# Optimization experiments

Measured on AMD Instinct MI355X. Metric: run time of the kernel, lower is better.

## Reference

```python
import jax, jax.numpy as jnp
import numpy as np

FEATS = 768
HEAD = 12
HD = FEATS // HEAD  # 64
B, N = 128, 197


def setup_inputs() -> dict:
    key = jax.random.key(0)
    k0, k1, k2 = jax.random.split(key, 3)
    x = jax.random.normal(k0, (B, N, FEATS), dtype=jnp.float32)
    W_qkv = jax.random.normal(k1, (HEAD, HD, 3 * HD), dtype=jnp.float32) * 0.05
    b_qkv = jnp.zeros((HEAD, 3 * HD), dtype=jnp.float32)
    # out_dim_3dk: Linear(feats -> feats)
    W_out = jax.random.normal(k2, (FEATS, FEATS), dtype=jnp.float32) * 0.02
    b_out = jnp.zeros((FEATS,), dtype=jnp.float32)
    return {"x": x, "W_qkv": W_qkv, "b_qkv": b_qkv, "W_out": W_out, "b_out": b_out}


def reference(x, W_qkv, b_qkv, W_out, b_out):
    b, n, f = x.shape
    h, hd = W_qkv.shape[0], W_qkv.shape[1]
    # x.chunk(head, dim=2) == reshape into per-head feature slices
    xh = x.reshape(b, n, h, hd)
    # per-head Linear(hd -> 3*hd): hX_dim_3dk
    qkv = jnp.einsum('bnhd,hde->bnhe', xh, W_qkv) + b_qkv  # [b,n,h,3*hd]
    q, k, v = jnp.split(qkv, 3, axis=-1)  # each [b,n,h,hd]
    # NOTE: original scales by sqrt(feats), not sqrt(head_dim)
    scale = jnp.asarray(f, x.dtype) ** 0.5
    scores = jnp.einsum('bihd,bjhd->bhij', q, k) / scale  # [b,h,n,n]
    p = jax.nn.softmax(scores, axis=-1)
    attn = jnp.einsum('bhij,bjhd->bihd', p, v)  # [b,n,h,hd]
    # concat head outputs along feature dim, then out_dim_3dk
    out = attn.reshape(b, n, f) @ W_out + b_out
    return out  # dropout p=0.0 is identity
```

## Files before the change

### kernel.cpp

```cpp
#include <hip/hip_runtime.h>
#include <hip/hip_bf16.h>

#define FEATS 768
#define HEADS 12
#define HD    64
#define BB    128
#define NN    197
#define M_TOT (BB * NN)
#define SCALE_INV (3.6084391824351615e-02f)
#define VS    216

typedef __bf16 bf16x8 __attribute__((ext_vector_type(8)));
typedef float  f32x4  __attribute__((ext_vector_type(4)));
typedef unsigned short u16x8 __attribute__((ext_vector_type(8)));

__device__ __forceinline__ unsigned short f2bf1(float f) {
    __bf16 h = (__bf16)f;
    return *(unsigned short*)&h;
}
__device__ __forceinline__ unsigned int f2bf2(float lo, float hi) {
    return (unsigned int)f2bf1(lo) | ((unsigned int)f2bf1(hi) << 16);
}

__global__ __launch_bounds__(256) void prep_kernel(
    const float* __restrict__ Wqkv, unsigned short* __restrict__ Wt_sw,
    const float* __restrict__ W,    unsigned short* __restrict__ Wt)
{
    __shared__ __align__(16) char plds[49152];
    const int t = threadIdx.x;
    if (blockIdx.x < 12) {
        float* wl = (float*)plds;
        const int h = blockIdx.x;
        const float* Wh = Wqkv + (long)h * (64 * 192);
        for (int i = t; i < 64 * 192; i += 256) wl[i] = Wh[i];
        __syncthreads();
        for (int c = t; c < 1536; c += 256) {
            int row = c >> 3, kc = (c & 7) ^ (row & 7);
            u16x8 v;
            #pragma unroll
            for (int j = 0; j < 8; ++j) v[j] = f2bf1(wl[(kc * 8 + j) * 192 + row]);
            *(u16x8*)&Wt_sw[(long)h * 12288 + c * 8] = v;
        }
    } else {
        float (*tile)[33] = (float(*)[33])plds;
        const int idx = blockIdx.x - 12;
        const int kb = (idx % 24) * 32, nb = (idx / 24) * 32;
        const int tx = t & 31, ty = t >> 5;
        for (int r = ty; r < 32; r += 8)
            tile[r][tx] = W[(long)(kb + r) * FEATS + nb + tx];
        __syncthreads();
        for (int r = ty; r < 32; r += 8) {
            const int n = nb + r, k = kb + tx;
            const long phys = (long)n * FEATS + ((k >> 6) << 6)
                            + ((((k >> 3) & 7) ^ (n & 7)) << 3) + (k & 7);
            Wt[phys] = f2bf1(tile[tx][r]);
        }
    }
}

__global__ __launch_bounds__(512, 4) void qkv_attn_fused(
    const float* __restrict__ x, const unsigned short* __restrict__ Wt_sw,
    const float* __restrict__ bqkv, unsigned short* __restrict__ attn)
{
    __shared__ __align__(16) char lds[80912];
    unsigned short* As  = (unsigned short*)lds;
    unsigned short* Ws  = (unsigned short*)(lds + 26624);
    unsigned short* Ql  = (unsigned short*)lds;
    unsigned short* Kl  = (unsigned short*)(lds + 26624);
    unsigned short* Vtl = (unsigned short*)(lds + 53248);
    unsigned short* Pl  = (unsigned short*)lds;

    const int t  = threadIdx.x;
    const int w  = t >> 6, l = t & 63;
    const int lr = l & 15, g = l >> 4, g4 = g * 4;
    const int b  = blockIdx.x, h = blockIdx.y;

    {
        const uint4 z = {0, 0, 0, 0};
        #pragma unroll
        for (int it = 0; it < 4; ++it) {
            int idx = it * 512 + t;
            if (idx < 1729) *(uint4*)&Vtl[idx * 8] = z;
        }
    }
    #pragma unroll
    for (int it = 0; it < 4; ++it) {
        int p = it * 512 + t;
        if (p < 1664) {
            int row = p >> 3, kc = (p & 7) ^ (row & 7);
            uint4 pk = {0, 0, 0, 0};
            if (row < NN) {
                const float* src = x + ((long)b * NN + row) * FEATS + h * HD + kc * 8;
                const float4 x0 = *(const float4*)src;
                const float4 x1 = *(const float4*)(src + 4);
                pk.x = f2bf2(x0.x, x0.y); pk.y = f2bf2(x0.z, x0.w);
                pk.z = f2bf2(x1.x, x1.y); pk.w = f2bf2(x1.z, x1.w);
            }
            *(uint4*)&As[p * 8] = pk;
        }
    }
    const unsigned short* Wh = Wt_sw + (long)h * 12288;
    #pragma unroll
    for (int it = 0; it < 3; ++it) {
        const int cb = it * 512 + w * 64;
        __builtin_amdgcn_global_load_lds(
            (const __attribute__((address_space(1))) void*)(Wh + (cb + l) * 8),
            (__attribute__((address_space(3))) void*)(Ws + cb * 8),
            16, 0, 0);
    }
    __syncthreads();

    const int wn0 = (w & 3) * 48;
    const int f0  = (w >> 2) * 7;
    const int nf_ = (w >> 2) ? 6 : 7;

    bf16x8 bfr[3][2];
    #pragma unroll
    for (int ni = 0; ni < 3; ++ni) {
        const int rn = wn0 + ni * 16 + lr;
        #pragma unroll
        for (int ks = 0; ks < 2; ++ks)
            bfr[ni][ks] = *(const bf16x8*)&Ws[(rn * 8 + ((ks * 4 + g) ^ (rn & 7))) * 8];
    }

    f32x4 acc[7][3];
    #pragma unroll
    for (int ni = 0; ni < 3; ++ni) {
        const int e0 = wn0 + ni * 16;
        if (e0 < 128) {
            const f32x4 bq = *(const f32x4*)&bqkv[h * 192 + e0 + g4];
            #pragma unroll
            for (int mi = 0; mi < 7; ++mi) acc[mi][ni] = bq;
        } else {
            const float bq = bqkv[h * 192 + e0 + lr];
            #pragma unroll
            for (int mi = 0; mi < 7; ++mi)
                #pragma unroll
                for (int r = 0; r < 4; ++r) acc[mi][ni][r] = bq;
        }
    }

    #pragma unroll
    for (int mi = 0; mi < 7; ++mi) {
        if (mi < nf_) {
            const int rA = (f0 + mi) * 16 + lr;
            bf16x8 a0 = *(const bf16x8*)&As[(rA * 8 + ((0 + g) ^ (rA & 7))) * 8];
            bf16x8 a1 = *(const bf16x8*)&As[(rA * 8 + ((4 + g) ^ (rA & 7))) * 8];
            #pragma unroll
            for (int ni = 0; ni < 3; ++ni) {
                const int e0 = wn0 + ni * 16;
                if (e0 < 128) {
                    acc[mi][ni] = __builtin_amdgcn_mfma_f32_16x16x32_bf16(
                        bfr[ni][0], a0, acc[mi][ni], 0, 0, 0);
                    acc[mi][ni] = __builtin_amdgcn_mfma_f32_16x16x32_bf16(
                        bfr[ni][1], a1, acc[mi][ni], 0, 0, 0);
                } else {
                    acc[mi][ni] = __builtin_amdgcn_mfma_f32_16x16x32_bf16(
                        a0, bfr[ni][0], acc[mi][ni], 0, 0, 0);
                    acc[mi][ni] = __builtin_amdgcn_mfma_f32_16x16x32_bf16(
                        a1, bfr[ni][1], acc[mi][ni], 0, 0, 0);
                }
            }
        }
    }
    __syncthreads();

    #pragma unroll
    for (int mi = 0; mi < 7; ++mi) {
        if (mi < nf_) {
            const int m = (f0 + mi) * 16 + lr;
            #pragma unroll
            for (int ni = 0; ni < 3; ++ni) {
                const int e0 = wn0 + ni * 16;
                uint2 pv;
                pv.x = f2bf2(acc[mi][ni][0], acc[mi][ni][1]);
                pv.y = f2bf2(acc[mi][ni][2], acc[mi][ni][3]);
                if (e0 < 64) {
                    const int c = ((e0 + g4) >> 3) ^ (m & 7);
                    *(uint2*)&Ql[(m * 8 + c) * 8 + (g4 & 7)] = pv;
                } else if (e0 < 128) {
                    const int e = e0 - 64 + g4;
                    const int c = (e >> 3) ^ (m & 7);
                    *(uint2*)&Kl[(m * 8 + c) * 8 + (g4 & 7)] = pv;
                } else {
                    const int d = e0 - 128 + lr;
                    const int n0 = (f0 + mi) * 16 + g4;
                    *(uint2*)&Vtl[d * VS + n0] = pv;
                }
            }
        }
    }
    __syncthreads();

    const int nm = (w < 5) ? 2 : 1;
    bf16x8 qf[2][2];
    #pragma unroll
    for (int mi = 0; mi < 2; ++mi) {
        if (mi == 0 || mi < nm) {
            const int lm = (w + mi * 8) * 16 + lr;
            #pragma unroll
            for (int ks = 0; ks < 2; ++ks)
                qf[mi][ks] = *(const bf16x8*)&Ql[(lm * 8 + ((ks * 4 + g) ^ (lm & 7))) * 8];
        }
    }
    __syncthreads();

    u16x8 ob;
    #pragma unroll
    for (int j = 0; j < 8; ++j) ob[j] = 0x3F80;
    bf16x8 onesf = *(bf16x8*)&ob;

    f32x4 oacc[2][4] = {};
    f32x4 ssum[2] = {};

    for (int tt = 0; tt < 7; ++tt) {
        const int kv0 = tt * 32;
        const int NF2 = (tt == 6) ? 1 : 2;

        bf16x8 kf[2][2];
        #pragma unroll
        for (int nf2 = 0; nf2 < 2; ++nf2) {
            if (nf2 < NF2) {
                const int row = kv0 + nf2 * 16 + lr;
                #pragma unroll
                for (int ks = 0; ks < 2; ++ks)
                    kf[nf2][ks] = *(const bf16x8*)&Kl[(row * 8 + ((ks * 4 + g) ^ (row & 7))) * 8];
            }
        }

        f32x4 s[2][2] = {};
        #pragma unroll
        for (int mi = 0; mi < 2; ++mi) {
            if (mi < nm) {
                #pragma unroll
                for (int nf2 = 0; nf2 < 2; ++nf2) {
                    if (nf2 < NF2) {
                        s[mi][nf2] = __builtin_amdgcn_mfma_f32_16x16x32_bf16(
                            qf[mi][0], kf[nf2][0], s[mi][nf2], 0, 0, 0);
                        s[mi][nf2] = __builtin_amdgcn_mfma_f32_16x16x32_bf16(
                            qf[mi][1], kf[nf2][1], s[mi][nf2], 0, 0, 0);
                    }
                }
            }
        }

        #pragma unroll
        for (int mi = 0; mi < 2; ++mi) {
            if (mi < nm) {
                #pragma unroll
                for (int nf2 = 0; nf2 < 2; ++nf2) {
                    const bool valid = (kv0 + nf2 * 16 + lr) < NN;
                    const int c = nf2 * 2 + (lr >> 3);
                    #pragma unroll
                    for (int r = 0; r < 4; ++r) {
                        float p = __expf(s[mi][nf2][r] * SCALE_INV);
                        p = valid ? p : 0.f;
                        const int q = (w + mi * 8) * 16 + g4 + r;
                        Pl[q * 40 + (c ^ g) * 8 + (lr & 7)] = f2bf1(p);
                    }
                }
            }
        }

        bf16x8 vf[4];
        #pragma unroll
        for (int df = 0; df < 4; ++df)
            vf[df] = *(const bf16x8*)&Vtl[(df * 16 + lr) * VS + kv0 + g * 8];
        #pragma unroll
        for (int mi = 0; mi < 2; ++mi) {
            if (mi < nm) {
                const int q = (w + mi * 8) * 16 + lr;
                bf16x8 pa = *(const bf16x8*)&Pl[q * 40 + (g ^ ((lr >> 2) & 3)) * 8];
                #pragma unroll
                for (int df = 0; df < 4; ++df)
                    oacc[mi][df] = __builtin_amdgcn_mfma_f32_16x16x32_bf16(
                        pa, vf[df], oacc[mi][df], 0, 0, 0);
                ssum[mi] = __builtin_amdgcn_mfma_f32_16x16x32_bf16(
                    pa, onesf, ssum[mi], 0, 0, 0);
            }
        }
    }

    #pragma unroll
    for (int mi = 0; mi < 2; ++mi) {
        if (mi < nm) {
            f32x4 inv;
            #pragma unroll
            for (int r = 0; r < 4; ++r) inv[r] = 1.0f / ssum[mi][r];
            #pragma unroll
            for (int df = 0; df < 4; ++df) {
                #pragma unroll
                for (int r = 0; r < 4; ++r) {
                    const int grow = (w + mi * 8) * 16 + g4 + r;
                    if (grow < NN) {
                        const long am = (long)b * NN + grow;
                        const int cc = (df * 2 + (lr >> 3)) ^ ((int)(am & 7));
                        attn[am * FEATS + h * HD + cc * 8 + (lr & 7)]
                            = f2bf1(oacc[mi][df][r] * inv[r]);
                    }
                }
            }
        }
    }
}

__global__ __launch_bounds__(256) void outproj_mfma(
    const unsigned short* __restrict__ A,
    const unsigned short* __restrict__ Bt,
    const float* __restrict__ bout, float* __restrict__ out)
{
    __shared__ unsigned short As2[128 * 64];
    __shared__ unsigned short Bs2[128 * 64];

    const int t  = threadIdx.x;
    const int w  = t >> 6;
    const int l  = t & 63;
    const int idx  = blockIdx.x;
    const int xcd  = idx & 7, qq = idx >> 3;
    const int start = (xcd < 6) ? xcd * 148 : 888 + (xcd - 6) * 147;
    const int wk = start + qq;
    const int m0 = (wk / 6) * 128;
    const int n0 = (wk % 6) * 128;
    const int wm = (w >> 1) * 64;
    const int wn = (w & 1) * 64;
    const int lr = l & 15;
    const int lk = l >> 4;
    const int l7 = lr & 7;

    f32x4 acc[4][4] = {};

    for (int k0 = 0; k0 < FEATS; k0 += 64) {
        #pragma unroll
        for (int c = 0; c < 4; ++c) {
            const int p   = c * 256 + t;
            const int row = p >> 3;
            const int col = (p & 7) * 8;
            __builtin_amdgcn_global_load_lds(
                (const __attribute__((address_space(1))) void*)
                    (A + (long)(m0 + row) * FEATS + k0 + col),
                (__attribute__((address_space(3))) void*)(As2 + (c * 256 + w * 64) * 8),
                16, 0, 0);
            __builtin_amdgcn_global_load_lds(
                (const __attribute__((address_space(1))) void*)
                    (Bt + (long)(n0 + row) * FEATS + k0 + col),
                (__attribute__((address_space(3))) void*)(Bs2 + (c * 256 + w * 64) * 8),
                16, 0, 0);
        }
        __syncthreads();

        #pragma unroll
        for (int s = 0; s < 2; ++s) {
            bf16x8 af[4], bfr[4];
            #pragma unroll
            for (int mi = 0; mi < 4; ++mi)
                af[mi] = *(const bf16x8*)(As2 + (wm + mi * 16 + lr) * 64
                                              + (((s * 4 + lk) ^ l7)) * 8);
            #pragma unroll
            for (int ni = 0; ni < 4; ++ni)
                bfr[ni] = *(const bf16x8*)(Bs2 + (wn + ni * 16 + lr) * 64
                                               + (((s * 4 + lk) ^ l7)) * 8);
            #pragma unroll
            for (int mi = 0; mi < 4; ++mi)
                #pragma unroll
                for (int ni = 0; ni < 4; ++ni)
                    acc[mi][ni] = __builtin_amdgcn_mfma_f32_16x16x32_bf16(
                        af[mi], bfr[ni], acc[mi][ni], 0, 0, 0);
        }
        __syncthreads();
    }

    float bv[4];
    #pragma unroll
    for (int ni = 0; ni < 4; ++ni) bv[ni] = bout[n0 + wn + ni * 16 + lr];
    #pragma unroll
    for (int mi = 0; mi < 4; ++mi) {
        #pragma unroll
        for (int ni = 0; ni < 4; ++ni) {
            const int gcol = n0 + wn + ni * 16 + lr;
            #pragma unroll
            for (int r = 0; r < 4; ++r) {
                const int grow = m0 + wm + mi * 16 + lk * 4 + r;
                out[(long)grow * FEATS + gcol] = acc[mi][ni][r] + bv[ni];
            }
        }
    }
}

extern "C" void kernel_launch(void* const* d_in, const int* in_sizes, int n_in,
                              void* d_out, int out_size, void* d_ws, size_t ws_size,
                              hipStream_t stream)
{
    const float* x    = (const float*)d_in[0];
    const float* Wqkv = (const float*)d_in[1];
    const float* bqkv = (const float*)d_in[2];
    const float* Wout = (const float*)d_in[3];
    const float* bout = (const float*)d_in[4];
    float* out = (float*)d_out;

    unsigned short* wsp = (unsigned short*)d_ws;
    const long S = (long)M_TOT * FEATS;
    unsigned short* attn  = wsp;
    unsigned short* Wt_sw = wsp + S;
    unsigned short* Wt    = wsp + S + 150000;

    prep_kernel<<<dim3(588), 256, 0, stream>>>(Wqkv, Wt_sw, Wout, Wt);

    qkv_attn_fused<<<dim3(BB, HEADS), 512, 0, stream>>>(x, Wt_sw, bqkv, attn);

    outproj_mfma<<<dim3(1182), 256, 0, stream>>>(attn, Wt, bout, out);
}
```

Measured before the change: 121.0 us.

## Shrink out-projection tiles to 64x128 with K=32 steps and drop XOR swizzle

The output-projection GEMM moves from 128x128 tiles with K-step 64 to 64x128 tiles with K-step 32, which doubles the grid to 2364 blocks. The XCD-aware block remap is adjusted to match. The XOR swizzle on the attention output and on the transposed W_out layout is removed, so both are now written row-major. The goal is more blocks for occupancy and load balance, at the cost of less reuse per tile, twice as many barriers per K, and possible LDS bank conflicts now that the swizzle is gone.

```diff
diff --git a/kernel.cpp b/kernel.cpp
--- a/kernel.cpp
+++ b/kernel.cpp
@@ -49,12 +49,8 @@
         for (int r = ty; r < 32; r += 8)
             tile[r][tx] = W[(long)(kb + r) * FEATS + nb + tx];
         __syncthreads();
-        for (int r = ty; r < 32; r += 8) {
-            const int n = nb + r, k = kb + tx;
-            const long phys = (long)n * FEATS + ((k >> 6) << 6)
-                            + ((((k >> 3) & 7) ^ (n & 7)) << 3) + (k & 7);
-            Wt[phys] = f2bf1(tile[tx][r]);
-        }
+        for (int r = ty; r < 32; r += 8)
+            Wt[(long)(nb + r) * FEATS + kb + tx] = f2bf1(tile[tx][r]);
     }
 }
 
@@ -292,12 +288,9 @@
                 #pragma unroll
                 for (int r = 0; r < 4; ++r) {
                     const int grow = (w + mi * 8) * 16 + g4 + r;
-                    if (grow < NN) {
-                        const long am = (long)b * NN + grow;
-                        const int cc = (df * 2 + (lr >> 3)) ^ ((int)(am & 7));
-                        attn[am * FEATS + h * HD + cc * 8 + (lr & 7)]
+                    if (grow < NN)
+                        attn[((long)b * NN + grow) * FEATS + h * HD + df * 16 + lr]
                             = f2bf1(oacc[mi][df][r] * inv[r]);
-                    }
                 }
             }
         }
@@ -309,37 +302,40 @@
     const unsigned short* __restrict__ Bt,
     const float* __restrict__ bout, float* __restrict__ out)
 {
-    __shared__ unsigned short As2[128 * 64];
-    __shared__ unsigned short Bs2[128 * 64];
+    __shared__ unsigned short As2[64 * 32];
+    __shared__ unsigned short Bs2[128 * 32];
 
     const int t  = threadIdx.x;
     const int w  = t >> 6;
     const int l  = t & 63;
-    const int idx  = blockIdx.x;
-    const int xcd  = idx & 7, qq = idx >> 3;
-    const int start = (xcd < 6) ? xcd * 148 : 888 + (xcd - 6) * 147;
-    const int wk = start + qq;
-    const int m0 = (wk / 6) * 128;
+    const int idx = blockIdx.x;
+    const int xcd = idx & 7, j = idx >> 3;
+    const int start = (xcd < 4) ? xcd * 296 : 1184 + (xcd - 4) * 295;
+    const int wk = start + j;
+    const int m0 = (wk / 6) * 64;
     const int n0 = (wk % 6) * 128;
-    const int wm = (w >> 1) * 64;
+    const int wm = (w >> 1) * 32;
     const int wn = (w & 1) * 64;
     const int lr = l & 15;
     const int lk = l >> 4;
-    const int l7 = lr & 7;
-
-    f32x4 acc[4][4] = {};
-
-    for (int k0 = 0; k0 < FEATS; k0 += 64) {
-        #pragma unroll
-        for (int c = 0; c < 4; ++c) {
-            const int p   = c * 256 + t;
-            const int row = p >> 3;
-            const int col = (p & 7) * 8;
+
+    f32x4 acc[2][4] = {};
+
+    for (int k0 = 0; k0 < FEATS; k0 += 32) {
+        {
+            const int row = t >> 2;
+            const int col = (t & 3) * 8;
             __builtin_amdgcn_global_load_lds(
                 (const __attribute__((address_space(1))) void*)
                     (A + (long)(m0 + row) * FEATS + k0 + col),
-                (__attribute__((address_space(3))) void*)(As2 + (c * 256 + w * 64) * 8),
+                (__attribute__((address_space(3))) void*)(As2 + w * 512),
                 16, 0, 0);
+        }
+        #pragma unroll
+        for (int c = 0; c < 2; ++c) {
+            const int p   = c * 256 + t;
+            const int row = p >> 2;
+            const int col = (p & 3) * 8;
             __builtin_amdgcn_global_load_lds(
                 (const __attribute__((address_space(1))) void*)
                     (Bt + (long)(n0 + row) * FEATS + k0 + col),
@@ -348,24 +344,19 @@
         }
         __syncthreads();
 
-        #pragma unroll
-        for (int s = 0; s < 2; ++s) {
-            bf16x8 af[4], bfr[4];
-            #pragma unroll
-            for (int mi = 0; mi < 4; ++mi)
-                af[mi] = *(const bf16x8*)(As2 + (wm + mi * 16 + lr) * 64
-                                              + (((s * 4 + lk) ^ l7)) * 8);
+        bf16x8 af[2], bfr[4];
+        #pragma unroll
+        for (int mi = 0; mi < 2; ++mi)
+            af[mi] = *(const bf16x8*)(As2 + (wm + mi * 16 + lr) * 32 + lk * 8);
+        #pragma unroll
+        for (int ni = 0; ni < 4; ++ni)
+            bfr[ni] = *(const bf16x8*)(Bs2 + (wn + ni * 16 + lr) * 32 + lk * 8);
+        #pragma unroll
+        for (int mi = 0; mi < 2; ++mi)
             #pragma unroll
             for (int ni = 0; ni < 4; ++ni)
-                bfr[ni] = *(const bf16x8*)(Bs2 + (wn + ni * 16 + lr) * 64
-                                               + (((s * 4 + lk) ^ l7)) * 8);
-            #pragma unroll
-            for (int mi = 0; mi < 4; ++mi)
-                #pragma unroll
-                for (int ni = 0; ni < 4; ++ni)
-                    acc[mi][ni] = __builtin_amdgcn_mfma_f32_16x16x32_bf16(
-                        af[mi], bfr[ni], acc[mi][ni], 0, 0, 0);
-        }
+                acc[mi][ni] = __builtin_amdgcn_mfma_f32_16x16x32_bf16(
+                    af[mi], bfr[ni], acc[mi][ni], 0, 0, 0);
         __syncthreads();
     }
 
@@ -373,7 +364,7 @@
     #pragma unroll
     for (int ni = 0; ni < 4; ++ni) bv[ni] = bout[n0 + wn + ni * 16 + lr];
     #pragma unroll
-    for (int mi = 0; mi < 4; ++mi) {
+    for (int mi = 0; mi < 2; ++mi) {
         #pragma unroll
         for (int ni = 0; ni < 4; ++ni) {
             const int gcol = n0 + wn + ni * 16 + lr;
@@ -407,5 +398,5 @@
 
     qkv_attn_fused<<<dim3(BB, HEADS), 512, 0, stream>>>(x, Wt_sw, bqkv, attn);
 
-    outproj_mfma<<<dim3(1182), 256, 0, stream>>>(attn, Wt, bout, out);
-}
+    outproj_mfma<<<dim3(2364), 256, 0, stream>>>(attn, Wt, bout, out);
+}
```

Measured after the change: 132.7 us. +9.7%, slower.
